# Optimization experiments

Measured on AMD Instinct MI355X. Metric: run time of the kernel, lower is better.

Reference implementation:

```python
import jax, jax.numpy as jnp
import numpy as np

B, S, H, FF, E, K, A = 2, 2048, 2048, 8192, 8, 2, 64
P = 3 * H * FF                      # num_ffn_params (gate + up + down)
NS = int(P * 1e-4)                  # num_sparse = 5033
TEMP = 1.0                          # mask_temperature


def setup_inputs() -> dict:
    key = jax.random.key(0)
    ks = jax.random.split(key, 9)
    f32 = jnp.float32
    return {
        "hidden_states": jax.random.normal(ks[0], (B, S, H), f32),
        "gate_w": jax.random.normal(ks[1], (FF, H), f32) * 0.02,
        "up_w": jax.random.normal(ks[2], (FF, H), f32) * 0.02,
        "down_w": jax.random.normal(ks[3], (H, FF), f32) * 0.02,
        "router_w": jax.random.normal(ks[4], (E, H), f32) * 0.01,
        "mask_logits": jax.random.normal(ks[5], (P,), f32) * 0.01,
        "atoms": jax.random.normal(ks[6], (A, NS), f32) * 0.02,
        "expert_atom_weights": jax.random.normal(ks[7], (E, A), f32) * 0.1,
        "importance": jax.random.normal(ks[8], (E, NS), f32) * 0.1,
    }


def reference(hidden_states, gate_w, up_w, down_w, router_w, mask_logits,
              atoms, expert_atom_weights, importance):
    b, s, h = hidden_states.shape
    x = hidden_states.reshape(-1, h)                      # (T, H) tokens

    # ---- SRDERouter: gate -> clamp -> top-k -> softmax over top-k ----
    router_logits = jnp.clip(x @ router_w.T, -50.0, 50.0)  # (T, E)
    top_w, top_idx = jax.lax.top_k(router_logits, K)       # (T, K)
    router_weights = jax.nn.softmax(top_w, axis=-1)        # (T, K)

    # ---- LearnedMaskSelector (eval path: no gumbel noise), straight-through ----
    noisy = jnp.clip(mask_logits / TEMP, -50.0, 50.0)      # (P,)
    soft_mask = jax.nn.sigmoid(noisy)
    _, mask_idx = jax.lax.top_k(noisy, NS)                 # (NS,) positions in param space
    hard_mask = jnp.zeros_like(soft_mask).at[mask_idx].set(1.0)
    mask = hard_mask - jax.lax.stop_gradient(soft_mask) + soft_mask  # (P,)

    # ---- SharedDeltaVocabulary + SparseExpert importance weighting ----
    atom_w = jax.nn.softmax(expert_atom_weights, axis=-1)  # (E, A)
    deltas = atom_w @ atoms                                # (E, NS)
    weighted_deltas = deltas * jax.nn.sigmoid(importance)  # (E, NS)

    # ---- per-token gather of top-k expert deltas, weighted combine ----
    tok_deltas = weighted_deltas[top_idx]                  # (T, K, NS) irregular gather
    combined = jnp.einsum('tk,tks->ts', router_weights, tok_deltas)  # (T, NS)
    mean_delta = combined.mean(axis=0)                     # (NS,) batch-averaged delta

    # ---- scatter sparse delta into flat FFN param space, apply mask ----
    flat = jnp.concatenate([gate_w.ravel(), up_w.ravel(), down_w.ravel()])  # (P,)
    delta_full = jnp.zeros_like(flat).at[mask_idx].set(mean_delta) * mask
    new_flat = flat + delta_full
    n1 = FF * H
    gw = new_flat[:n1].reshape(FF, H)
    uw = new_flat[n1:2 * n1].reshape(FF, H)
    dw = new_flat[2 * n1:].reshape(H, FF)

    # ---- SwiGLU FFN with delta-perturbed params ----
    hidden = jax.nn.silu(x @ gw.T) * (x @ uw.T)            # (T, FF)
    out = (hidden @ dw.T).reshape(b, s, h)

    # ---- load-balancing aux loss ----
    probs = jax.nn.softmax(router_logits, axis=-1)         # (T, E)
    frac = jax.nn.one_hot(top_idx, E, dtype=probs.dtype).sum(1).mean(0) / K  # (E,)
    aux_loss = E * jnp.sum(probs.mean(0) * frac)

    return out, router_logits, router_weights, top_idx, aux_loss
```

## Files before the change

kernel.cpp:

```cpp
#include <hip/hip_runtime.h>
#include <stdint.h>

#define DEV __device__ __forceinline__

typedef __attribute__((ext_vector_type(8))) short short8;
typedef __attribute__((ext_vector_type(4))) float f32x4;

constexpr int       Td  = 4096;
constexpr int       Hd  = 2048;
constexpr int       FFd = 8192;
constexpr int       NSd = 5033;
constexpr long long n1  = 16777216LL;
constexpr long long Pn  = 50331648LL;
constexpr int CAND_CAP = 8192;
constexpr unsigned DUMP_CAP = 131072;
constexpr unsigned KEY_DUMP = 0xBCF5C28Fu;
constexpr unsigned BIN_BASE = KEY_DUMP >> 18;
constexpr int      NB2      = 16384 - (int)BIN_BASE;
constexpr int      NSB      = (NB2 + 63) / 64;

constexpr size_t OUT_LOGITS = 8388608;
constexpr size_t OUT_RW     = 8421376;
constexpr size_t OUT_TI     = 8429568;
constexpr size_t OUT_AUX    = 8437760;

constexpr size_t OFF_W    = 0;
constexpr size_t OFF_X    = 100663296;
constexpr size_t OFF_HID  = 117440512;
constexpr size_t OFF_META = 184549376;
constexpr size_t OFF_CAND = OFF_META + 256;
constexpr size_t OFF_MIDX = OFF_CAND + CAND_CAP * 8;
constexpr size_t OFF_MD   = OFF_MIDX + 20480;

DEV unsigned short f2bf(float f) {
    unsigned u = __float_as_uint(f);
    u += 0x7FFFu + ((u >> 16) & 1u);
    return (unsigned short)(u >> 16);
}
DEV unsigned keyof(float v) {
    v = fminf(50.f, fmaxf(-50.f, v));
    unsigned b = __float_as_uint(v);
    return (b & 0x80000000u) ? ~b : (b | 0x80000000u);
}

#define GL16(gsrc, ldst) __builtin_amdgcn_global_load_lds( \
    (const __attribute__((address_space(1))) unsigned int*)(const void*)(gsrc), \
    (__attribute__((address_space(3))) unsigned int*)(void*)(ldst), 16, 0, 0)

#define SWZC(r, c) ((c) ^ (((r) & 7) << 3))
#define SWZ(r, c)  (((r) * 64) + SWZC(r, c))

#define MFMA16 __builtin_amdgcn_mfma_f32_16x16x32_bf16
#define LGKM(n) do { asm volatile("s_waitcnt lgkmcnt(" #n ")" ::: "memory"); \
                     __builtin_amdgcn_sched_barrier(0); } while (0)

__global__ __launch_bounds__(256) void k_cvt_w(const float4* __restrict__ g,
                                               const float4* __restrict__ u,
                                               const float4* __restrict__ d,
                                               ushort4* __restrict__ o) {
    const long long n1_4 = n1 / 4, n4 = Pn / 4;
    long long stride = (long long)gridDim.x * blockDim.x;
    for (long long i = blockIdx.x * (long long)blockDim.x + threadIdx.x; i < n4; i += stride) {
        float4 v = (i < n1_4) ? g[i] : (i < 2 * n1_4) ? u[i - n1_4] : d[i - 2 * n1_4];
        ushort4 r; r.x = f2bf(v.x); r.y = f2bf(v.y); r.z = f2bf(v.z); r.w = f2bf(v.w);
        o[i] = r;
    }
}

__global__ __launch_bounds__(1024) void k_router(const float* __restrict__ x,
                                                 const float* __restrict__ rw,
                                                 float* __restrict__ out,
                                                 float* __restrict__ meta_f,
                                                 ushort4* __restrict__ xbf) {
    __shared__ float sacc[24];
    int tid = threadIdx.x;
    if (tid < 24) sacc[tid] = 0.f;
    __syncthreads();
    int wid = tid >> 6, lane = tid & 63;
    int t = blockIdx.x * 16 + wid;
    const float4* xr = (const float4*)(x + (size_t)t * Hd);
    ushort4* xw = xbf + (size_t)t * (Hd / 4);
    double acc[8] = {0, 0, 0, 0, 0, 0, 0, 0};
    for (int i = 0; i < 8; ++i) {
        float4 xv = xr[i * 64 + lane];
        ushort4 xc; xc.x = f2bf(xv.x); xc.y = f2bf(xv.y); xc.z = f2bf(xv.z); xc.w = f2bf(xv.w);
        xw[i * 64 + lane] = xc;
#pragma unroll
        for (int e = 0; e < 8; ++e) {
            float4 wv = ((const float4*)(rw + (size_t)e * Hd))[i * 64 + lane];
            acc[e] += (double)xv.x * wv.x + (double)xv.y * wv.y +
                      (double)xv.z * wv.z + (double)xv.w * wv.w;
        }
    }
#pragma unroll
    for (int e = 0; e < 8; ++e)
        for (int s = 32; s; s >>= 1) acc[e] += __shfl_xor(acc[e], s, 64);
    if (lane == 0) {
        float lg[8];
#pragma unroll
        for (int e = 0; e < 8; ++e) lg[e] = fminf(50.f, fmaxf(-50.f, (float)acc[e]));
        float* lo = out + OUT_LOGITS + (size_t)t * 8;
#pragma unroll
        for (int e = 0; e < 8; ++e) lo[e] = lg[e];
        int i1 = 0;
        for (int e = 1; e < 8; ++e) if (lg[e] > lg[i1]) i1 = e;
        int i2 = (i1 == 0) ? 1 : 0;
        for (int e = 0; e < 8; ++e) if (e != i1 && lg[e] > lg[i2]) i2 = e;
        float e2 = expf(lg[i2] - lg[i1]);
        float r1 = 1.f / (1.f + e2), r2 = e2 / (1.f + e2);
        out[OUT_RW + (size_t)t * 2]     = r1;
        out[OUT_RW + (size_t)t * 2 + 1] = r2;
        out[OUT_TI + (size_t)t * 2]     = (float)i1;
        out[OUT_TI + (size_t)t * 2 + 1] = (float)i2;
        float m = lg[0];
        for (int e = 1; e < 8; ++e) m = fmaxf(m, lg[e]);
        float p[8], s = 0.f;
#pragma unroll
        for (int e = 0; e < 8; ++e) { p[e] = expf(lg[e] - m); s += p[e]; }
        float inv = 1.f / s;
        atomicAdd(&sacc[i1], r1);  atomicAdd(&sacc[i2], r2);
        atomicAdd(&sacc[8 + i1], 1.f); atomicAdd(&sacc[8 + i2], 1.f);
#pragma unroll
        for (int e = 0; e < 8; ++e) atomicAdd(&sacc[16 + e], p[e] * inv);
    }
    __syncthreads();
    if (tid < 24) atomicAdd(&meta_f[4 + tid], sacc[tid]);
}

__global__ __launch_bounds__(256) void k_dump(const float4* __restrict__ ml,
                                              unsigned* __restrict__ meta_u,
                                              unsigned long long* __restrict__ cand2) {
    __shared__ unsigned long long buf[1024];
    __shared__ unsigned cnt, base;
    if (threadIdx.x == 0) cnt = 0;
    __syncthreads();
    const long long n4 = Pn / 4;
    long long stride = (long long)gridDim.x * 256;
    for (long long i = blockIdx.x * 256LL + threadIdx.x; i < n4; i += stride) {
        float4 v = ml[i];
        float vv[4] = {v.x, v.y, v.z, v.w};
#pragma unroll
        for (int j = 0; j < 4; ++j) {
            unsigned k = keyof(vv[j]);
            if (k >= KEY_DUMP) {
                unsigned p = atomicAdd(&cnt, 1u);
                if (p < 1024)
                    buf[p] = ((unsigned long long)k << 32) |
                             (unsigned)~(unsigned)(i * 4 + j);
            }
        }
    }
    __syncthreads();
    if (threadIdx.x == 0) {
        unsigned c = cnt; if (c > 1024) c = 1024;
        base = atomicAdd(&meta_u[2], c);
        cnt = c;
    }
    __syncthreads();
    for (unsigned i = threadIdx.x; i < cnt; i += 256)
        if (base + i < DUMP_CAP) cand2[base + i] = buf[i];
}

__global__ __launch_bounds__(1024) void k_hist2(const unsigned long long* __restrict__ cand2,
                                                unsigned* __restrict__ meta_u) {
    __shared__ unsigned hh[NB2];
    __shared__ unsigned ssum[NSB], sabove[NSB];
    int tid = threadIdx.x;
    for (int i = tid; i < NB2; i += 1024) hh[i] = 0;
    __syncthreads();
    unsigned M2 = meta_u[2]; if (M2 > DUMP_CAP) M2 = DUMP_CAP;
    for (unsigned i = tid; i < M2; i += 1024)
        atomicAdd(&hh[(unsigned)(cand2[i] >> 50) - BIN_BASE], 1u);
    __syncthreads();
    if (tid < NSB) {
        unsigned s = 0;
        int hi = tid * 64 + 64; if (hi > NB2) hi = NB2;
        for (int b = tid * 64; b < hi; ++b) s += hh[b];
        ssum[tid] = s;
    }
    __syncthreads();
    if (tid == 0) {
        unsigned run = 0;
        for (int i = NSB - 1; i >= 0; --i) { sabove[i] = run; run += ssum[i]; }
    }
    __syncthreads();
    if (tid < NSB) {
        unsigned above = sabove[tid];
        if (above < (unsigned)NSd && above + ssum[tid] >= (unsigned)NSd) {
            unsigned cum = above;
            int hi = tid * 64 + 64; if (hi > NB2) hi = NB2;
            for (int b = hi - 1; b >= tid * 64; --b) {
                cum += hh[b];
                if (cum >= (unsigned)NSd) { meta_u[1] = (unsigned)b + BIN_BASE; break; }
            }
        }
    }
}

__global__ __launch_bounds__(256) void k_collect(const unsigned long long* __restrict__ cand2,
                                                 unsigned* __restrict__ meta_u,
                                                 unsigned long long* __restrict__ cand) {
    unsigned M2 = meta_u[2]; if (M2 > DUMP_CAP) M2 = DUMP_CAP;
    unsigned i = blockIdx.x * 256 + threadIdx.x;
    if (i < M2) {
        unsigned long long c = cand2[i];
        if ((unsigned)(c >> 50) >= meta_u[1]) {
            unsigned pos = atomicAdd(&meta_u[0], 1u);
            if (pos < CAND_CAP) cand[pos] = c;
        }
    }
}

__global__ __launch_bounds__(1024) void k_sort(const unsigned* __restrict__ meta_u,
                                               const unsigned long long* __restrict__ cand,
                                               unsigned* __restrict__ midx) {
    __shared__ unsigned long long sh[CAND_CAP];
    unsigned M = meta_u[0]; if (M > CAND_CAP) M = CAND_CAP;
    for (int i = threadIdx.x; i < CAND_CAP; i += 1024) sh[i] = (i < (int)M) ? cand[i] : 0ULL;
    __syncthreads();
    for (int k = 2; k <= CAND_CAP; k <<= 1)
        for (int j = k >> 1; j > 0; j >>= 1) {
            for (int i = threadIdx.x; i < CAND_CAP; i += 1024) {
                int l = i ^ j;
                if (l > i) {
                    unsigned long long a = sh[i], b = sh[l];
                    bool up = ((i & k) == 0);
                    if ((a > b) == up) { sh[i] = b; sh[l] = a; }
                }
            }
            __syncthreads();
        }
    for (int r = threadIdx.x; r < NSd; r += 1024)
        midx[r] = ~(unsigned)sh[CAND_CAP - 1 - r];
}

__global__ __launch_bounds__(256) void k_delta(const float* __restrict__ atoms,
                                               const float* __restrict__ eaw,
                                               const float* __restrict__ imp,
                                               const float* __restrict__ meta_f,
                                               float* __restrict__ md,
                                               float* __restrict__ out) {
    __shared__ float aw[8][64];
    int tid = threadIdx.x;
    if (tid < 8) {
        float m = -1e30f;
        for (int a = 0; a < 64; ++a) m = fmaxf(m, eaw[tid * 64 + a]);
        float s = 0.f;
        for (int a = 0; a < 64; ++a) { float v = expf(eaw[tid * 64 + a] - m); aw[tid][a] = v; s += v; }
        float inv = 1.f / s;
        for (int a = 0; a < 64; ++a) aw[tid][a] *= inv;
    }
    __syncthreads();
    int s_ = blockIdx.x * 256 + tid;
    if (s_ < NSd) {
        float d[8] = {0, 0, 0, 0, 0, 0, 0, 0};
        for (int a = 0; a < 64; ++a) {
            float av = atoms[(size_t)a * NSd + s_];
#pragma unroll
            for (int e = 0; e < 8; ++e) d[e] += aw[e][a] * av;
        }
        float m = 0.f;
#pragma unroll
        for (int e = 0; e < 8; ++e) {
            float coef = meta_f[4 + e] * (1.f / Td);
            float sg = 1.f / (1.f + expf(-imp[(size_t)e * NSd + s_]));
            m += coef * d[e] * sg;
        }
        md[s_] = m;
    }
    if (blockIdx.x == 0 && tid == 0) {
        float aux = 0.f;
        for (int e = 0; e < 8; ++e)
            aux += (meta_f[20 + e] / Td) * (meta_f[12 + e] / (Td * 2.f));
        out[OUT_AUX] = 8.f * aux;
    }
}

__global__ __launch_bounds__(256) void k_scatter(const unsigned* __restrict__ midx,
                                                 const float* __restrict__ md,
                                                 const float* __restrict__ g,
                                                 const float* __restrict__ u,
                                                 const float* __restrict__ dn,
                                                 unsigned short* __restrict__ wsW) {
    int i = blockIdx.x * 256 + threadIdx.x;
    if (i >= NSd) return;
    long long pos = (long long)midx[i];
    float orig = (pos < n1) ? g[pos] : (pos < 2 * n1) ? u[pos - n1] : dn[pos - 2 * n1];
    wsW[pos] = f2bf(orig + md[i]);
}

__global__ __launch_bounds__(512, 2) void k_gemm_gu(const unsigned short* __restrict__ Abf,
                                                    const unsigned short* __restrict__ Wg,
                                                    const unsigned short* __restrict__ Wu,
                                                    unsigned short* __restrict__ Hid) {
    extern __shared__ unsigned short sm[];
    const int tid = threadIdx.x, wid = tid >> 6, lane = tid & 63;
    const int lr = lane & 15, ko = (lane >> 4) * 8;
    const int wm = wid >> 2, wn = wid & 3;
    const int orig = blockIdx.x;
    const int swz = (orig & 7) * 128 + (orig >> 3);
    const int bm = swz & 15, bn = swz >> 4;
    const size_t arow = (size_t)bm * 256;
    const size_t brow = (size_t)bn * 128;

    f32x4 ag[8][2], au[8][2];
#pragma unroll
    for (int i = 0; i < 8; ++i)
#pragma unroll
        for (int j = 0; j < 2; ++j) { ag[i][j] = (f32x4)0.f; au[i][j] = (f32x4)0.f; }

    auto ST_A0 = [&](int kt, int b) {
        const int k0 = kt * 64; unsigned short* L = sm + b * 32768;
#pragma unroll
        for (int i = 0; i < 2; ++i) { int e = (i * 512 + tid) * 8; int r = e >> 6, c = e & 63;
            GL16(Abf + (arow + r) * 2048 + k0 + SWZC(r, c), L + e); } };
    auto ST_A1 = [&](int kt, int b) {
        const int k0 = kt * 64; unsigned short* L = sm + b * 32768;
#pragma unroll
        for (int i = 0; i < 2; ++i) { int e = 8192 + (i * 512 + tid) * 8; int r = e >> 6, c = e & 63;
            GL16(Abf + (arow + r) * 2048 + k0 + SWZC(r, c), L + e); } };
    auto ST_BG = [&](int kt, int b) {
        const int k0 = kt * 64; unsigned short* L = sm + b * 32768;
#pragma unroll
        for (int i = 0; i < 2; ++i) { int e = (i * 512 + tid) * 8; int r = e >> 6, c = e & 63;
            GL16(Wg + (brow + r) * 2048 + k0 + SWZC(r, c), L + 16384 + e); } };
    auto ST_BU = [&](int kt, int b) {
        const int k0 = kt * 64; unsigned short* L = sm + b * 32768;
#pragma unroll
        for (int i = 0; i < 2; ++i) { int e = (i * 512 + tid) * 8; int r = e >> 6, c = e & 63;
            GL16(Wu + (brow + r) * 2048 + k0 + SWZC(r, c), L + 24576 + e); } };

    constexpr int NT = 2048 / 64;
    ST_A0(0, 0); ST_A1(0, 0); ST_BG(0, 0); ST_BU(0, 0); ST_A0(1, 1); ST_A1(1, 1);
    for (int t = 0; t < NT; ++t) {
        const int cur = t & 1, nb = cur ^ 1;
        unsigned short* L = sm + cur * 32768;
        if (t + 1 < NT) asm volatile("s_waitcnt vmcnt(4)" ::: "memory");
        else            asm volatile("s_waitcnt vmcnt(0)" ::: "memory");
        __builtin_amdgcn_s_barrier();
        short8 a0[8], a1[8], bg[2][2], bu[2][2];
#pragma unroll
        for (int m = 0; m < 8; ++m) a0[m] = *(const short8*)&L[SWZ(wm * 128 + m * 16 + lr, ko)];
        bg[0][0] = *(const short8*)&L[16384 + SWZ(wn * 32 + lr, ko)];
        bg[1][0] = *(const short8*)&L[16384 + SWZ(wn * 32 + 16 + lr, ko)];
        if (t + 1 < NT) ST_BG(t + 1, nb);
#pragma unroll
        for (int m = 0; m < 8; ++m) a1[m] = *(const short8*)&L[SWZ(wm * 128 + m * 16 + lr, 32 + ko)];
        bg[0][1] = *(const short8*)&L[16384 + SWZ(wn * 32 + lr, 32 + ko)];
        bg[1][1] = *(const short8*)&L[16384 + SWZ(wn * 32 + 16 + lr, 32 + ko)];
        if (t + 1 < NT) ST_BU(t + 1, nb);
        LGKM(10);
        __builtin_amdgcn_s_setprio(1);
#pragma unroll
        for (int m = 0; m < 8; ++m) {
            ag[m][0] = MFMA16(a0[m], bg[0][0], ag[m][0], 0, 0, 0);
            ag[m][1] = MFMA16(a0[m], bg[1][0], ag[m][1], 0, 0, 0);
        }
        __builtin_amdgcn_s_setprio(0);
        bu[0][0] = *(const short8*)&L[24576 + SWZ(wn * 32 + lr, ko)];
        bu[1][0] = *(const short8*)&L[24576 + SWZ(wn * 32 + 16 + lr, ko)];
        LGKM(2);
        __builtin_amdgcn_s_barrier();
        if (t + 2 < NT) { ST_A0(t + 2, cur); ST_A1(t + 2, cur); }
        __builtin_amdgcn_s_setprio(1);
#pragma unroll
        for (int m = 0; m < 8; ++m) {
            ag[m][0] = MFMA16(a1[m], bg[0][1], ag[m][0], 0, 0, 0);
            ag[m][1] = MFMA16(a1[m], bg[1][1], ag[m][1], 0, 0, 0);
        }
        __builtin_amdgcn_s_setprio(0);
        bu[0][1] = *(const short8*)&L[24576 + SWZ(wn * 32 + lr, 32 + ko)];
        bu[1][1] = *(const short8*)&L[24576 + SWZ(wn * 32 + 16 + lr, 32 + ko)];
        LGKM(2);
        __builtin_amdgcn_s_setprio(1);
#pragma unroll
        for (int m = 0; m < 8; ++m) {
            au[m][0] = MFMA16(a0[m], bu[0][0], au[m][0], 0, 0, 0);
            au[m][1] = MFMA16(a0[m], bu[1][0], au[m][1], 0, 0, 0);
        }
        __builtin_amdgcn_s_setprio(0);
        LGKM(0);
        __builtin_amdgcn_s_setprio(1);
#pragma unroll
        for (int m = 0; m < 8; ++m) {
            au[m][0] = MFMA16(a1[m], bu[0][1], au[m][0], 0, 0, 0);
            au[m][1] = MFMA16(a1[m], bu[1][1], au[m][1], 0, 0, 0);
        }
        __builtin_amdgcn_s_setprio(0);
    }
    const int rbase = (int)arow + wm * 128 + (lane >> 4) * 4;
    const int cbase = (int)brow + wn * 32 + lr;
#pragma unroll
    for (int mf = 0; mf < 8; ++mf)
#pragma unroll
        for (int nf = 0; nf < 2; ++nf)
#pragma unroll
            for (int reg = 0; reg < 4; ++reg) {
                float gv = ag[mf][nf][reg], uv = au[mf][nf][reg];
                float h = gv / (1.f + expf(-gv)) * uv;
                Hid[(size_t)(rbase + mf * 16 + reg) * FFd + cbase + nf * 16] = f2bf(h);
            }
}

__global__ __launch_bounds__(512, 2) void k_gemm_dn(const unsigned short* __restrict__ Abf,
                                                    const unsigned short* __restrict__ Wd,
                                                    float* __restrict__ Out) {
    extern __shared__ unsigned short sm[];
    const int tid = threadIdx.x, wid = tid >> 6, lane = tid & 63;
    const int lr = lane & 15, ko = (lane >> 4) * 8;
    const int wm = wid >> 2, wn = wid & 3;
    const int orig = blockIdx.x;
    const int swz = (orig & 7) * 32 + (orig >> 3);
    const int bn = swz & 7, bm = swz >> 3;
    const size_t arow = (size_t)bm * 128;
    const size_t brow = (size_t)bn * 256;

    f32x4 acc[4][4];
#pragma unroll
    for (int i = 0; i < 4; ++i)
#pragma unroll
        for (int j = 0; j < 4; ++j) acc[i][j] = (f32x4)0.f;

    auto ST_A = [&](int kt, int b) {
        const int k0 = kt * 64; unsigned short* L = sm + b * 24576;
#pragma unroll
        for (int i = 0; i < 2; ++i) { int e = (i * 512 + tid) * 8; int r = e >> 6, c = e & 63;
            GL16(Abf + (arow + r) * 8192 + k0 + SWZC(r, c), L + e); } };
    auto ST_B = [&](int kt, int b) {
        const int k0 = kt * 64; unsigned short* L = sm + b * 24576;
#pragma unroll
        for (int i = 0; i < 4; ++i) { int e = (i * 512 + tid) * 8; int r = e >> 6, c = e & 63;
            GL16(Wd + (brow + r) * 8192 + k0 + SWZC(r, c), L + 8192 + e); } };

    constexpr int NT = 8192 / 64;
    ST_A(0, 0); ST_B(0, 0); ST_A(1, 1); ST_B(1, 1);
    int cur = 0;
    for (int t = 0; t < NT; ++t) {
        unsigned short* L = sm + cur * 24576;
        const int b2 = (cur + 2 >= 3) ? cur - 1 : cur + 2;
        if (t + 1 < NT) asm volatile("s_waitcnt vmcnt(6)" ::: "memory");
        else            asm volatile("s_waitcnt vmcnt(0)" ::: "memory");
        __builtin_amdgcn_s_barrier();
        short8 a[4][2], b0[4], b1[4];
#pragma unroll
        for (int m = 0; m < 4; ++m)
            a[m][0] = *(const short8*)&L[SWZ(wm * 64 + m * 16 + lr, ko)];
#pragma unroll
        for (int n = 0; n < 4; ++n)
            b0[n] = *(const short8*)&L[8192 + SWZ(wn * 64 + n * 16 + lr, ko)];
#pragma unroll
        for (int m = 0; m < 4; ++m)
            a[m][1] = *(const short8*)&L[SWZ(wm * 64 + m * 16 + lr, 32 + ko)];
#pragma unroll
        for (int n = 0; n < 4; ++n)
            b1[n] = *(const short8*)&L[8192 + SWZ(wn * 64 + n * 16 + lr, 32 + ko)];
        if (t + 2 < NT) { ST_B(t + 2, b2); ST_A(t + 2, b2); }
        LGKM(8);
        __builtin_amdgcn_s_setprio(1);
#pragma unroll
        for (int m = 0; m < 4; ++m)
#pragma unroll
            for (int n = 0; n < 4; ++n)
                acc[m][n] = MFMA16(a[m][0], b0[n], acc[m][n], 0, 0, 0);
        __builtin_amdgcn_s_setprio(0);
        LGKM(0);
        __builtin_amdgcn_s_setprio(1);
#pragma unroll
        for (int m = 0; m < 4; ++m)
#pragma unroll
            for (int n = 0; n < 4; ++n)
                acc[m][n] = MFMA16(a[m][1], b1[n], acc[m][n], 0, 0, 0);
        __builtin_amdgcn_s_setprio(0);
        cur = (cur + 1 >= 3) ? 0 : cur + 1;
    }
    const int rbase = (int)arow + wm * 64 + (lane >> 4) * 4;
    const int cbase = (int)brow + wn * 64 + lr;
#pragma unroll
    for (int mf = 0; mf < 4; ++mf)
#pragma unroll
        for (int nf = 0; nf < 4; ++nf)
#pragma unroll
            for (int reg = 0; reg < 4; ++reg)
                Out[(size_t)(rbase + mf * 16 + reg) * Hd + cbase + nf * 16] = acc[mf][nf][reg];
}

extern "C" void kernel_launch(void* const* d_in, const int* in_sizes, int n_in,
                              void* d_out, int out_size, void* d_ws, size_t ws_size,
                              hipStream_t stream) {
    const float* x     = (const float*)d_in[0];
    const float* gate  = (const float*)d_in[1];
    const float* up    = (const float*)d_in[2];
    const float* down  = (const float*)d_in[3];
    const float* rw    = (const float*)d_in[4];
    const float* ml    = (const float*)d_in[5];
    const float* atoms = (const float*)d_in[6];
    const float* eaw   = (const float*)d_in[7];
    const float* imp   = (const float*)d_in[8];
    float* out = (float*)d_out;
    char*  ws  = (char*)d_ws;

    unsigned short* wsW  = (unsigned short*)(ws + OFF_W);
    unsigned short* xbf  = (unsigned short*)(ws + OFF_X);
    unsigned short* hid  = (unsigned short*)(ws + OFF_HID);
    unsigned*       mu   = (unsigned*)(ws + OFF_META);
    float*          mf   = (float*)(ws + OFF_META);
    unsigned long long* cand = (unsigned long long*)(ws + OFF_CAND);
    unsigned*       midx = (unsigned*)(ws + OFF_MIDX);
    float*          md   = (float*)(ws + OFF_MD);
    unsigned long long* cand2 = (unsigned long long*)(ws + OFF_HID);

    hipFuncSetAttribute((const void*)k_gemm_gu,
                        hipFuncAttributeMaxDynamicSharedMemorySize, 131072);
    hipFuncSetAttribute((const void*)k_gemm_dn,
                        hipFuncAttributeMaxDynamicSharedMemorySize, 147456);

    hipMemsetAsync(ws + OFF_META, 0, 256, stream);

    k_cvt_w<<<4096, 256, 0, stream>>>((const float4*)gate, (const float4*)up,
                                      (const float4*)down, (ushort4*)wsW);
    k_router<<<Td / 16, 1024, 0, stream>>>(x, rw, out, mf, (ushort4*)xbf);
    k_dump<<<1024, 256, 0, stream>>>((const float4*)ml, mu, cand2);
    k_hist2<<<1, 1024, 0, stream>>>(cand2, mu);
    k_collect<<<512, 256, 0, stream>>>(cand2, mu, cand);
    k_sort<<<1, 1024, 0, stream>>>(mu, cand, midx);
    k_delta<<<(NSd + 255) / 256, 256, 0, stream>>>(atoms, eaw, imp, mf, md, out);
    k_scatter<<<(NSd + 255) / 256, 256, 0, stream>>>(midx, md, gate, up, down, wsW);
    k_gemm_gu<<<1024, 512, 131072, stream>>>(xbf, wsW, wsW + n1, hid);
    k_gemm_dn<<<256, 512, 147456, stream>>>(hid, wsW + 2 * n1, out);
}
```

Baseline: 653.9 us.

## Switch FFN GEMMs to 32x32x16 MFMA and stage epilogues through LDS

Both the gate/up GEMM and the down-projection GEMM move from 16x16x32 bf16 MFMA tiles to 32x32x16 tiles, with the LDS fragment loads and accumulators rearranged to match. This reduces the number of LDS fragment reads per FLOP and the instruction count per K-step. The epilogues now write results into shared memory first, then issue coalesced vector stores to global memory instead of scattered scalar stores. The cost is more accumulator registers per tile and an extra barrier plus an LDS round-trip at the end of each block.

After: 707.5 us. 1.08x slower.

```diff
diff --git a/kernel.cpp b/kernel.cpp
--- a/kernel.cpp
+++ b/kernel.cpp
@@ -5,6 +5,7 @@
 
 typedef __attribute__((ext_vector_type(8))) short short8;
 typedef __attribute__((ext_vector_type(4))) float f32x4;
+typedef __attribute__((ext_vector_type(16))) float f32x16;
 
 constexpr int       Td  = 4096;
 constexpr int       Hd  = 2048;
@@ -50,7 +51,7 @@
 #define SWZC(r, c) ((c) ^ (((r) & 7) << 3))
 #define SWZ(r, c)  (((r) * 64) + SWZC(r, c))
 
-#define MFMA16 __builtin_amdgcn_mfma_f32_16x16x32_bf16
+#define MFMA32 __builtin_amdgcn_mfma_f32_32x32x16_bf16
 #define LGKM(n) do { asm volatile("s_waitcnt lgkmcnt(" #n ")" ::: "memory"); \
                      __builtin_amdgcn_sched_barrier(0); } while (0)
 
@@ -295,7 +296,7 @@
                                                     unsigned short* __restrict__ Hid) {
     extern __shared__ unsigned short sm[];
     const int tid = threadIdx.x, wid = tid >> 6, lane = tid & 63;
-    const int lr = lane & 15, ko = (lane >> 4) * 8;
+    const int lr = lane & 31, ko = (lane >> 5) * 8;
     const int wm = wid >> 2, wn = wid & 3;
     const int orig = blockIdx.x;
     const int swz = (orig & 7) * 128 + (orig >> 3);
@@ -303,11 +304,9 @@
     const size_t arow = (size_t)bm * 256;
     const size_t brow = (size_t)bn * 128;
 
-    f32x4 ag[8][2], au[8][2];
-#pragma unroll
-    for (int i = 0; i < 8; ++i)
-#pragma unroll
-        for (int j = 0; j < 2; ++j) { ag[i][j] = (f32x4)0.f; au[i][j] = (f32x4)0.f; }
+    f32x16 ag[4], au[4];
+#pragma unroll
+    for (int i = 0; i < 4; ++i) { ag[i] = (f32x16)0.f; au[i] = (f32x16)0.f; }
 
     auto ST_A0 = [&](int kt, int b) {
         const int k0 = kt * 64; unsigned short* L = sm + b * 32768;
@@ -338,68 +337,78 @@
         if (t + 1 < NT) asm volatile("s_waitcnt vmcnt(4)" ::: "memory");
         else            asm volatile("s_waitcnt vmcnt(0)" ::: "memory");
         __builtin_amdgcn_s_barrier();
-        short8 a0[8], a1[8], bg[2][2], bu[2][2];
-#pragma unroll
-        for (int m = 0; m < 8; ++m) a0[m] = *(const short8*)&L[SWZ(wm * 128 + m * 16 + lr, ko)];
-        bg[0][0] = *(const short8*)&L[16384 + SWZ(wn * 32 + lr, ko)];
-        bg[1][0] = *(const short8*)&L[16384 + SWZ(wn * 32 + 16 + lr, ko)];
+        short8 a[4][4], bg[4], bu[4];
+#pragma unroll
+        for (int m = 0; m < 4; ++m) a[m][0] = *(const short8*)&L[SWZ(wm * 128 + m * 32 + lr, ko)];
+#pragma unroll
+        for (int m = 0; m < 4; ++m) a[m][1] = *(const short8*)&L[SWZ(wm * 128 + m * 32 + lr, 16 + ko)];
+        bg[0] = *(const short8*)&L[16384 + SWZ(wn * 32 + lr, ko)];
+        bg[1] = *(const short8*)&L[16384 + SWZ(wn * 32 + lr, 16 + ko)];
         if (t + 1 < NT) ST_BG(t + 1, nb);
 #pragma unroll
-        for (int m = 0; m < 8; ++m) a1[m] = *(const short8*)&L[SWZ(wm * 128 + m * 16 + lr, 32 + ko)];
-        bg[0][1] = *(const short8*)&L[16384 + SWZ(wn * 32 + lr, 32 + ko)];
-        bg[1][1] = *(const short8*)&L[16384 + SWZ(wn * 32 + 16 + lr, 32 + ko)];
+        for (int m = 0; m < 4; ++m) a[m][2] = *(const short8*)&L[SWZ(wm * 128 + m * 32 + lr, 32 + ko)];
+#pragma unroll
+        for (int m = 0; m < 4; ++m) a[m][3] = *(const short8*)&L[SWZ(wm * 128 + m * 32 + lr, 48 + ko)];
+        bg[2] = *(const short8*)&L[16384 + SWZ(wn * 32 + lr, 32 + ko)];
+        bg[3] = *(const short8*)&L[16384 + SWZ(wn * 32 + lr, 48 + ko)];
         if (t + 1 < NT) ST_BU(t + 1, nb);
         LGKM(10);
         __builtin_amdgcn_s_setprio(1);
 #pragma unroll
-        for (int m = 0; m < 8; ++m) {
-            ag[m][0] = MFMA16(a0[m], bg[0][0], ag[m][0], 0, 0, 0);
-            ag[m][1] = MFMA16(a0[m], bg[1][0], ag[m][1], 0, 0, 0);
+        for (int m = 0; m < 4; ++m) {
+            ag[m] = MFMA32(a[m][0], bg[0], ag[m], 0, 0, 0);
+            ag[m] = MFMA32(a[m][1], bg[1], ag[m], 0, 0, 0);
         }
         __builtin_amdgcn_s_setprio(0);
-        bu[0][0] = *(const short8*)&L[24576 + SWZ(wn * 32 + lr, ko)];
-        bu[1][0] = *(const short8*)&L[24576 + SWZ(wn * 32 + 16 + lr, ko)];
+        bu[0] = *(const short8*)&L[24576 + SWZ(wn * 32 + lr, ko)];
+        bu[1] = *(const short8*)&L[24576 + SWZ(wn * 32 + lr, 16 + ko)];
         LGKM(2);
         __builtin_amdgcn_s_barrier();
         if (t + 2 < NT) { ST_A0(t + 2, cur); ST_A1(t + 2, cur); }
         __builtin_amdgcn_s_setprio(1);
 #pragma unroll
-        for (int m = 0; m < 8; ++m) {
-            ag[m][0] = MFMA16(a1[m], bg[0][1], ag[m][0], 0, 0, 0);
-            ag[m][1] = MFMA16(a1[m], bg[1][1], ag[m][1], 0, 0, 0);
+        for (int m = 0; m < 4; ++m) {
+            ag[m] = MFMA32(a[m][2], bg[2], ag[m], 0, 0, 0);
+            ag[m] = MFMA32(a[m][3], bg[3], ag[m], 0, 0, 0);
         }
         __builtin_amdgcn_s_setprio(0);
-        bu[0][1] = *(const short8*)&L[24576 + SWZ(wn * 32 + lr, 32 + ko)];
-        bu[1][1] = *(const short8*)&L[24576 + SWZ(wn * 32 + 16 + lr, 32 + ko)];
+        bu[2] = *(const short8*)&L[24576 + SWZ(wn * 32 + lr, 32 + ko)];
+        bu[3] = *(const short8*)&L[24576 + SWZ(wn * 32 + lr, 48 + ko)];
         LGKM(2);
         __builtin_amdgcn_s_setprio(1);
 #pragma unroll
-        for (int m = 0; m < 8; ++m) {
-            au[m][0] = MFMA16(a0[m], bu[0][0], au[m][0], 0, 0, 0);
-            au[m][1] = MFMA16(a0[m], bu[1][0], au[m][1], 0, 0, 0);
+        for (int m = 0; m < 4; ++m) {
+            au[m] = MFMA32(a[m][0], bu[0], au[m], 0, 0, 0);
+            au[m] = MFMA32(a[m][1], bu[1], au[m], 0, 0, 0);
         }
         __builtin_amdgcn_s_setprio(0);
         LGKM(0);
         __builtin_amdgcn_s_setprio(1);
 #pragma unroll
-        for (int m = 0; m < 8; ++m) {
-            au[m][0] = MFMA16(a1[m], bu[0][1], au[m][0], 0, 0, 0);
-            au[m][1] = MFMA16(a1[m], bu[1][1], au[m][1], 0, 0, 0);
+        for (int m = 0; m < 4; ++m) {
+            au[m] = MFMA32(a[m][2], bu[2], au[m], 0, 0, 0);
+            au[m] = MFMA32(a[m][3], bu[3], au[m], 0, 0, 0);
         }
         __builtin_amdgcn_s_setprio(0);
     }
-    const int rbase = (int)arow + wm * 128 + (lane >> 4) * 4;
-    const int cbase = (int)brow + wn * 32 + lr;
-#pragma unroll
-    for (int mf = 0; mf < 8; ++mf)
-#pragma unroll
-        for (int nf = 0; nf < 2; ++nf)
-#pragma unroll
-            for (int reg = 0; reg < 4; ++reg) {
-                float gv = ag[mf][nf][reg], uv = au[mf][nf][reg];
-                float h = gv / (1.f + expf(-gv)) * uv;
-                Hid[(size_t)(rbase + mf * 16 + reg) * FFd + cbase + nf * 16] = f2bf(h);
-            }
+    __builtin_amdgcn_s_barrier();
+#pragma unroll
+    for (int m = 0; m < 4; ++m)
+#pragma unroll
+        for (int reg = 0; reg < 16; ++reg) {
+            int r = wm * 128 + m * 32 + (reg & 3) + 8 * (reg >> 2) + 4 * (lane >> 5);
+            int c = wn * 32 + lr;
+            float gv = ag[m][reg], uv = au[m][reg];
+            float h = gv / (1.f + expf(-gv)) * uv;
+            sm[r * 136 + c] = f2bf(h);
+        }
+    __syncthreads();
+#pragma unroll
+    for (int p = 0; p < 8; ++p) {
+        int r = p * 32 + (tid >> 4), c = (tid & 15) * 8;
+        short8 v = *(const short8*)&sm[r * 136 + c];
+        *(short8*)&Hid[(arow + r) * (size_t)FFd + brow + c] = v;
+    }
 }
 
 __global__ __launch_bounds__(512, 2) void k_gemm_dn(const unsigned short* __restrict__ Abf,
@@ -407,7 +416,7 @@
                                                     float* __restrict__ Out) {
     extern __shared__ unsigned short sm[];
     const int tid = threadIdx.x, wid = tid >> 6, lane = tid & 63;
-    const int lr = lane & 15, ko = (lane >> 4) * 8;
+    const int lr = lane & 31, ko = (lane >> 5) * 8;
     const int wm = wid >> 2, wn = wid & 3;
     const int orig = blockIdx.x;
     const int swz = (orig & 7) * 32 + (orig >> 3);
@@ -415,11 +424,11 @@
     const size_t arow = (size_t)bm * 128;
     const size_t brow = (size_t)bn * 256;
 
-    f32x4 acc[4][4];
-#pragma unroll
-    for (int i = 0; i < 4; ++i)
-#pragma unroll
-        for (int j = 0; j < 4; ++j) acc[i][j] = (f32x4)0.f;
+    f32x16 acc[2][2];
+#pragma unroll
+    for (int i = 0; i < 2; ++i)
+#pragma unroll
+        for (int j = 0; j < 2; ++j) acc[i][j] = (f32x16)0.f;
 
     auto ST_A = [&](int kt, int b) {
         const int k0 = kt * 64; unsigned short* L = sm + b * 24576;
@@ -441,47 +450,69 @@
         if (t + 1 < NT) asm volatile("s_waitcnt vmcnt(6)" ::: "memory");
         else            asm volatile("s_waitcnt vmcnt(0)" ::: "memory");
         __builtin_amdgcn_s_barrier();
-        short8 a[4][2], b0[4], b1[4];
-#pragma unroll
-        for (int m = 0; m < 4; ++m)
-            a[m][0] = *(const short8*)&L[SWZ(wm * 64 + m * 16 + lr, ko)];
-#pragma unroll
-        for (int n = 0; n < 4; ++n)
-            b0[n] = *(const short8*)&L[8192 + SWZ(wn * 64 + n * 16 + lr, ko)];
-#pragma unroll
-        for (int m = 0; m < 4; ++m)
-            a[m][1] = *(const short8*)&L[SWZ(wm * 64 + m * 16 + lr, 32 + ko)];
-#pragma unroll
-        for (int n = 0; n < 4; ++n)
-            b1[n] = *(const short8*)&L[8192 + SWZ(wn * 64 + n * 16 + lr, 32 + ko)];
+        short8 a[2][4], b[2][4];
+#pragma unroll
+        for (int m = 0; m < 2; ++m) {
+            a[m][0] = *(const short8*)&L[SWZ(wm * 64 + m * 32 + lr, ko)];
+            a[m][1] = *(const short8*)&L[SWZ(wm * 64 + m * 32 + lr, 16 + ko)];
+        }
+#pragma unroll
+        for (int n = 0; n < 2; ++n) {
+            b[n][0] = *(const short8*)&L[8192 + SWZ(wn * 64 + n * 32 + lr, ko)];
+            b[n][1] = *(const short8*)&L[8192 + SWZ(wn * 64 + n * 32 + lr, 16 + ko)];
+        }
+#pragma unroll
+        for (int m = 0; m < 2; ++m) {
+            a[m][2] = *(const short8*)&L[SWZ(wm * 64 + m * 32 + lr, 32 + ko)];
+            a[m][3] = *(const short8*)&L[SWZ(wm * 64 + m * 32 + lr, 48 + ko)];
+        }
+#pragma unroll
+        for (int n = 0; n < 2; ++n) {
+            b[n][2] = *(const short8*)&L[8192 + SWZ(wn * 64 + n * 32 + lr, 32 + ko)];
+            b[n][3] = *(const short8*)&L[8192 + SWZ(wn * 64 + n * 32 + lr, 48 + ko)];
+        }
         if (t + 2 < NT) { ST_B(t + 2, b2); ST_A(t + 2, b2); }
         LGKM(8);
         __builtin_amdgcn_s_setprio(1);
 #pragma unroll
-        for (int m = 0; m < 4; ++m)
-#pragma unroll
-            for (int n = 0; n < 4; ++n)
-                acc[m][n] = MFMA16(a[m][0], b0[n], acc[m][n], 0, 0, 0);
+        for (int m = 0; m < 2; ++m)
+#pragma unroll
+            for (int n = 0; n < 2; ++n) {
+                acc[m][n] = MFMA32(a[m][0], b[n][0], acc[m][n], 0, 0, 0);
+                acc[m][n] = MFMA32(a[m][1], b[n][1], acc[m][n], 0, 0, 0);
+            }
         __builtin_amdgcn_s_setprio(0);
         LGKM(0);
         __builtin_amdgcn_s_setprio(1);
 #pragma unroll
-        for (int m = 0; m < 4; ++m)
-#pragma unroll
-            for (int n = 0; n < 4; ++n)
-                acc[m][n] = MFMA16(a[m][1], b1[n], acc[m][n], 0, 0, 0);
+        for (int m = 0; m < 2; ++m)
+#pragma unroll
+            for (int n = 0; n < 2; ++n) {
+                acc[m][n] = MFMA32(a[m][2], b[n][2], acc[m][n], 0, 0, 0);
+                acc[m][n] = MFMA32(a[m][3], b[n][3], acc[m][n], 0, 0, 0);
+            }
         __builtin_amdgcn_s_setprio(0);
         cur = (cur + 1 >= 3) ? 0 : cur + 1;
     }
-    const int rbase = (int)arow + wm * 64 + (lane >> 4) * 4;
-    const int cbase = (int)brow + wn * 64 + lr;
-#pragma unroll
-    for (int mf = 0; mf < 4; ++mf)
-#pragma unroll
-        for (int nf = 0; nf < 4; ++nf)
-#pragma unroll
-            for (int reg = 0; reg < 4; ++reg)
-                Out[(size_t)(rbase + mf * 16 + reg) * Hd + cbase + nf * 16] = acc[mf][nf][reg];
+    __builtin_amdgcn_s_barrier();
+    float* Lf = (float*)sm;
+#pragma unroll
+    for (int m = 0; m < 2; ++m)
+#pragma unroll
+        for (int n = 0; n < 2; ++n)
+#pragma unroll
+            for (int reg = 0; reg < 16; ++reg) {
+                int r = wm * 64 + m * 32 + (reg & 3) + 8 * (reg >> 2) + 4 * (lane >> 5);
+                int c = wn * 64 + n * 32 + lr;
+                Lf[r * 256 + c] = acc[m][n][reg];
+            }
+    __syncthreads();
+#pragma unroll
+    for (int p = 0; p < 16; ++p) {
+        int r = p * 8 + (tid >> 6), c = (tid & 63) * 4;
+        f32x4 v = *(const f32x4*)&Lf[r * 256 + c];
+        *(f32x4*)&Out[(arow + r) * (size_t)Hd + brow + c] = v;
+    }
 }
 
 extern "C" void kernel_launch(void* const* d_in, const int* in_sizes, int n_in,
```
